# Optimization experiments

Measured on AMD Instinct MI355X. Metric: run time of the kernel, lower is better.

Reference implementation:

```python
import jax, jax.numpy as jnp
import numpy as np

N = 40000   # nodes
D = 128     # hidden_dim
R = 8       # num_rels
E = 640000  # edges (avg degree 16)
ND = 4000   # diseases (sim_matrix rows)


def setup_inputs() -> dict:
    key = jax.random.key(0)
    ks = jax.random.split(key, 9)
    s = 1.0 / np.sqrt(D)
    x = jax.random.normal(ks[0], (N, D), dtype=jnp.float32)
    edge_src = jax.random.randint(ks[1], (E,), 0, N, dtype=jnp.int32)
    edge_dst = jax.random.randint(ks[2], (E,), 0, N, dtype=jnp.int32)
    edge_type = jax.random.randint(ks[3], (E,), 0, R, dtype=jnp.int32)
    sim_matrix = jax.random.uniform(ks[4], (ND, ND), dtype=jnp.float32)
    # Full-batch case: batch_n_id = arange(N); diseases are ND unique global node ids.
    # The torch forward derives local positions + sim-matrix rows from global2local;
    # with identity batch ids this reduces to the sorted disease ids and arange(ND).
    rng = np.random.default_rng(0)
    disease_glob = np.sort(rng.choice(N, size=ND, replace=False))
    batch_loc_indices = jnp.asarray(disease_glob, dtype=jnp.int32)
    matrix_row_indices = jnp.arange(ND, dtype=jnp.int32)
    W1_self = jax.random.normal(ks[5], (D, D), dtype=jnp.float32) * s
    W1_rel = jax.random.normal(ks[6], (R, D, D), dtype=jnp.float32) * s
    W2_self = jax.random.normal(ks[7], (D, D), dtype=jnp.float32) * s
    W2_rel = jax.random.normal(ks[8], (R, D, D), dtype=jnp.float32) * s
    return {
        "x": x, "sim_matrix": sim_matrix,
        "W1_self": W1_self, "W1_rel": W1_rel,
        "W2_self": W2_self, "W2_rel": W2_rel,
        "edge_src": edge_src, "edge_dst": edge_dst, "edge_type": edge_type,
        "batch_loc_indices": batch_loc_indices,
        "matrix_row_indices": matrix_row_indices,
    }


def _rgcn_layer(h, src, dst, etype, Wself, Wrel):
    # Per-(dst, relation) mean aggregation of neighbor features, then per-relation GEMM.
    seg = dst * R + etype                                        # [E]
    msg = jax.ops.segment_sum(h[src], seg, num_segments=N * R)   # [N*R, D]
    cnt = jax.ops.segment_sum(jnp.ones((src.shape[0],), h.dtype), seg,
                              num_segments=N * R)                # [N*R]
    agg = (msg / jnp.maximum(cnt, 1.0)[:, None]).reshape(N, R, h.shape[1])
    return h @ Wself + jnp.einsum('nrd,rdh->nh', agg, Wrel)


def reference(x, sim_matrix, W1_self, W1_rel, W2_self, W2_rel,
              edge_src, edge_dst, edge_type, batch_loc_indices, matrix_row_indices):
    # --- RGCN encoder (2 layers) ---
    h = jax.nn.relu(_rgcn_layer(x, edge_src, edge_dst, edge_type, W1_self, W1_rel))
    h = _rgcn_layer(h, edge_src, edge_dst, edge_type, W2_self, W2_rel)

    # --- similarity diffusion post-processing ---
    deg = jax.ops.segment_sum(jnp.ones((edge_src.shape[0],), h.dtype),
                              edge_dst, num_segments=N)          # in-degree [N]
    c = 0.7 * jnp.exp(-0.7 * deg)[:, None] + 0.2                 # [N,1]

    hb = h[batch_loc_indices]                                    # [ND, D]
    sim_sub = sim_matrix[matrix_row_indices][:, matrix_row_indices]
    sim_norm = sim_sub / (sim_sub.sum(axis=1, keepdims=True) + 1e-9)
    h_sim = sim_norm @ hb                                        # [ND, D]

    c_sub = c[batch_loc_indices]
    h_aug = c_sub * h_sim + (1.0 - c_sub) * hb
    return h.at[batch_loc_indices].set(h_aug)
```

## Files before the change

### kernel.cpp

```cpp
#include <hip/hip_runtime.h>
#include <hip/hip_bf16.h>

#define DD 128
#define RR 8
#define KK 1152
#define SCAN_CHUNK 2048
#define KSPLIT 8
#define KP 4096

typedef _Float16 h8 __attribute__((ext_vector_type(8)));
typedef _Float16 h4 __attribute__((ext_vector_type(4)));
typedef float f4 __attribute__((ext_vector_type(4)));

__device__ __forceinline__ void gload16(const _Float16* g, _Float16* l) {
  __builtin_amdgcn_global_load_lds(
      (const __attribute__((address_space(1))) void*)g,
      (__attribute__((address_space(3))) void*)l, 16, 0, 0);
}

__global__ __launch_bounds__(256) void count_k(const int* __restrict__ edst,
    const int* __restrict__ etyp, int* __restrict__ cnt, int E) {
  int i = blockIdx.x * 256 + threadIdx.x;
  if (i < E) atomicAdd(&cnt[edst[i] * RR + etyp[i]], 1);
}

__global__ __launch_bounds__(256) void scan_a(const int* __restrict__ cnt,
    int* __restrict__ off, int* __restrict__ bsum, int n) {
  __shared__ int red[256];
  int base = blockIdx.x * SCAN_CHUNK + threadIdx.x * 8;
  int v[8];
  int s = 0;
#pragma unroll
  for (int i = 0; i < 8; ++i) {
    int idx = base + i;
    v[i] = s;
    s += (idx < n) ? cnt[idx] : 0;
  }
  red[threadIdx.x] = s;
  __syncthreads();
  for (int o = 1; o < 256; o <<= 1) {
    int t = (threadIdx.x >= o) ? red[threadIdx.x - o] : 0;
    __syncthreads();
    red[threadIdx.x] += t;
    __syncthreads();
  }
  int pre = (threadIdx.x > 0) ? red[threadIdx.x - 1] : 0;
#pragma unroll
  for (int i = 0; i < 8; ++i) {
    int idx = base + i;
    if (idx < n) off[idx] = v[i] + pre;
  }
  if (threadIdx.x == 255) bsum[blockIdx.x] = red[255];
}

__global__ void scan_b(int* __restrict__ bsum, int nb) {
  if (threadIdx.x == 0) {
    int s = 0;
    for (int i = 0; i < nb; ++i) { int t = bsum[i]; bsum[i] = s; s += t; }
  }
}

__global__ __launch_bounds__(256) void scan_c(int* __restrict__ off,
    const int* __restrict__ bsum, int n) {
  int i = blockIdx.x * 256 + threadIdx.x;
  if (i < n) off[i] += bsum[i >> 11];
}

__global__ __launch_bounds__(256) void fill_k(const int* __restrict__ esrc,
    const int* __restrict__ edst, const int* __restrict__ etyp,
    int* __restrict__ cur, int* __restrict__ eidx, int E) {
  int e = blockIdx.x * 256 + threadIdx.x;
  if (e < E) {
    int seg = edst[e] * RR + etyp[e];
    int p = atomicAdd(&cur[seg], 1);
    eidx[p] = esrc[e];
  }
}

__global__ __launch_bounds__(256) void convx_k(const float* __restrict__ x,
    _Float16* __restrict__ xh, int n4) {
  int i = blockIdx.x * 256 + threadIdx.x;
  if (i < n4) {
    float4 v = *(const float4*)(x + (size_t)i * 4);
    h4 o = {(_Float16)v.x, (_Float16)v.y, (_Float16)v.z, (_Float16)v.w};
    *(h4*)(xh + (size_t)i * 4) = o;
  }
}

__global__ __launch_bounds__(256) void convwT_k(const float* __restrict__ Ws,
    const float* __restrict__ Wr, _Float16* __restrict__ WT) {
  __shared__ _Float16 tile[64][72];
  const int k0 = blockIdx.x * 64, n0 = blockIdx.y * 64;
  const int t = threadIdx.x;
  {
    int kr = t >> 2, c0 = (t & 3) * 16;
    int k = k0 + kr;
    const float* src = (k < DD) ? (Ws + (size_t)k * DD + n0 + c0)
                                : (Wr + (size_t)(k - DD) * DD + n0 + c0);
#pragma unroll
    for (int j = 0; j < 16; j += 4) {
      float4 v = *(const float4*)(src + j);
      tile[kr][c0 + j + 0] = (_Float16)v.x;
      tile[kr][c0 + j + 1] = (_Float16)v.y;
      tile[kr][c0 + j + 2] = (_Float16)v.z;
      tile[kr][c0 + j + 3] = (_Float16)v.w;
    }
  }
  __syncthreads();
  {
    int nr = t >> 2, ck = (t & 3) * 16;
    h8 o0, o1;
#pragma unroll
    for (int j = 0; j < 8; ++j) {
      o0[j] = tile[ck + j][nr];
      o1[j] = tile[ck + 8 + j][nr];
    }
    *(h8*)(WT + (size_t)(n0 + nr) * KK + k0 + ck) = o0;
    *(h8*)(WT + (size_t)(n0 + nr) * KK + k0 + ck + 8) = o1;
  }
}

__device__ __forceinline__ void agg_body(const _Float16* __restrict__ h,
    const int* __restrict__ off, const int* __restrict__ eidx,
    _Float16* __restrict__ msg, int nseg, int E, int gid) {
  int seg = gid >> 4, q = gid & 15;
  if (seg >= nseg) return;
  int b = off[seg];
  int e = (seg + 1 < nseg) ? off[seg + 1] : E;
  int n = e - b;
  float a[8];
#pragma unroll
  for (int j = 0; j < 8; ++j) a[j] = 0.f;
  if (n > 0) {
    int e1 = e - 1;
    int s0 = eidx[b];
    int s1 = eidx[min(b + 1, e1)];
    int s2 = eidx[min(b + 2, e1)];
    int s3 = eidx[min(b + 3, e1)];
    h8 v0 = *(const h8*)(h + (size_t)s0 * DD + q * 8);
    h8 v1 = *(const h8*)(h + (size_t)s1 * DD + q * 8);
    h8 v2 = *(const h8*)(h + (size_t)s2 * DD + q * 8);
    h8 v3 = *(const h8*)(h + (size_t)s3 * DD + q * 8);
#pragma unroll
    for (int j = 0; j < 8; ++j) a[j] = (float)v0[j];
    if (n > 1) {
#pragma unroll
      for (int j = 0; j < 8; ++j) a[j] += (float)v1[j];
    }
    if (n > 2) {
#pragma unroll
      for (int j = 0; j < 8; ++j) a[j] += (float)v2[j];
    }
    if (n > 3) {
#pragma unroll
      for (int j = 0; j < 8; ++j) a[j] += (float)v3[j];
    }
    for (int i = b + 4; i < e; ++i) {
      int s = eidx[i];
      h8 v = *(const h8*)(h + (size_t)s * DD + q * 8);
#pragma unroll
      for (int j = 0; j < 8; ++j) a[j] += (float)v[j];
    }
  }
  float ic = (n > 0) ? 1.0f / (float)n : 0.0f;
  h8 o;
#pragma unroll
  for (int j = 0; j < 8; ++j) o[j] = (_Float16)(a[j] * ic);
  *(h8*)(msg + (size_t)seg * DD + q * 8) = o;
}

__global__ __launch_bounds__(256) void agg_k(const _Float16* __restrict__ h,
    const int* __restrict__ off, const int* __restrict__ eidx,
    _Float16* __restrict__ msg, int nseg, int E) {
  agg_body(h, off, eidx, msg, nseg, E, blockIdx.x * 256 + threadIdx.x);
}

__device__ __forceinline__ void convsim_body(const float* __restrict__ sim,
    const int* __restrict__ mri, const float* __restrict__ maskf,
    _Float16* __restrict__ simh, float* __restrict__ rs, int nd, int i,
    float* red) {
  const float* row = sim + (size_t)mri[i] * nd;
  float acc = 0.f;
  for (int c4 = threadIdx.x; c4 < KP / 4; c4 += 256) {
    int c = c4 * 4;
    float4 v = make_float4(0.f, 0.f, 0.f, 0.f);
    if (c < nd) {
      v = *(const float4*)(row + c);
      float4 mk = *(const float4*)(maskf + c);
      acc += v.x * mk.x + v.y * mk.y + v.z * mk.z + v.w * mk.w;
    }
    h4 o = {(_Float16)v.x, (_Float16)v.y, (_Float16)v.z, (_Float16)v.w};
    *(h4*)(simh + (size_t)i * KP + c) = o;
  }
  red[threadIdx.x] = acc;
  __syncthreads();
  for (int o = 128; o > 0; o >>= 1) {
    if (threadIdx.x < o) red[threadIdx.x] += red[threadIdx.x + o];
    __syncthreads();
  }
  if (threadIdx.x == 0) rs[i] = red[0] + 1e-9f;
}

__global__ __launch_bounds__(256) void agg1_convsim_k(
    const _Float16* __restrict__ h, const int* __restrict__ off,
    const int* __restrict__ eidx, _Float16* __restrict__ msg, int nseg, int E,
    const float* __restrict__ sim, const int* __restrict__ mri,
    const float* __restrict__ maskf, _Float16* __restrict__ simh,
    float* __restrict__ rs, int nd) {
  __shared__ float red[256];
  if ((int)blockIdx.x < nd) {
    convsim_body(sim, mri, maskf, simh, rs, nd, blockIdx.x, red);
  } else {
    agg_body(h, off, eidx, msg, nseg, E,
             (blockIdx.x - nd) * 256 + threadIdx.x);
  }
}

template <bool RELU, bool F16OUT>
__global__ __launch_bounds__(256) void rgcn_mfma(const _Float16* __restrict__ xh,
    const _Float16* __restrict__ msg, const _Float16* __restrict__ WT,
    void* __restrict__ outv, int nN) {
  __shared__ _Float16 Ab[2][64 * 64];
  __shared__ _Float16 Bb[2][128 * 64];
  const int t = threadIdx.x;
  const int lane = t & 63, w = t >> 6;
  const int row0 = blockIdx.x * 64;
  const int wm = w >> 1, wn = w & 1;
  const int lr = lane & 15, lg = lane >> 4;

  f4 acc[2][4];
#pragma unroll
  for (int mi = 0; mi < 2; ++mi)
#pragma unroll
    for (int ni = 0; ni < 4; ++ni) acc[mi][ni] = (f4){0.f, 0.f, 0.f, 0.f};

  const _Float16* pxh[2];
  const _Float16* pmsg[2];
  int ldsA[2];
#pragma unroll
  for (int j = 0; j < 2; ++j) {
    int q = j * 256 + w * 64 + lane;
    int row = q >> 3;
    int gck = (q & 7) ^ (row & 7);
    int m = row0 + row; if (m >= nN) m = nN - 1;
    pxh[j] = xh + (size_t)m * DD + gck * 8;
    pmsg[j] = msg + (size_t)m * (RR * DD) + gck * 8;
    ldsA[j] = (j * 256 + w * 64) * 8;
  }
  const _Float16* pB[4];
  int ldsB[4];
#pragma unroll
  for (int i = 0; i < 4; ++i) {
    int q = i * 256 + w * 64 + lane;
    int n = q >> 3;
    int gck = (q & 7) ^ (n & 7);
    pB[i] = WT + (size_t)n * KK + gck * 8;
    ldsB[i] = (i * 256 + w * 64) * 8;
  }

  const int nsteps = KK / 64;
#pragma unroll
  for (int j = 0; j < 2; ++j) gload16(pxh[j], &Ab[0][ldsA[j]]);
#pragma unroll
  for (int i = 0; i < 4; ++i) gload16(pB[i], &Bb[0][ldsB[i]]);
  asm volatile("s_waitcnt vmcnt(0)" ::: "memory");
  __syncthreads();

  for (int ts = 0; ts < nsteps; ++ts) {
    const int cur = ts & 1;
    if (ts + 1 < nsteps) {
      const int kk = (ts + 1) * 64;
      const int nxt = cur ^ 1;
      if (kk < DD) {
#pragma unroll
        for (int j = 0; j < 2; ++j) gload16(pxh[j] + kk, &Ab[nxt][ldsA[j]]);
      } else {
#pragma unroll
        for (int j = 0; j < 2; ++j) gload16(pmsg[j] + (kk - DD), &Ab[nxt][ldsA[j]]);
      }
#pragma unroll
      for (int i = 0; i < 4; ++i) gload16(pB[i] + kk, &Bb[nxt][ldsB[i]]);
    }
#pragma unroll
    for (int s = 0; s < 2; ++s) {
      h8 af[2], bf[4];
#pragma unroll
      for (int mi = 0; mi < 2; ++mi) {
        int r = wm * 32 + mi * 16 + lr;
        af[mi] = *(const h8*)&Ab[cur][r * 64 + (((s * 4 + lg) ^ (r & 7)) << 3)];
      }
#pragma unroll
      for (int ni = 0; ni < 4; ++ni) {
        int n = wn * 64 + ni * 16 + lr;
        bf[ni] = *(const h8*)&Bb[cur][n * 64 + (((s * 4 + lg) ^ (n & 7)) << 3)];
      }
#pragma unroll
      for (int mi = 0; mi < 2; ++mi)
#pragma unroll
        for (int ni = 0; ni < 4; ++ni)
          acc[mi][ni] = __builtin_amdgcn_mfma_f32_16x16x32_f16(
              af[mi], bf[ni], acc[mi][ni], 0, 0, 0);
    }
    asm volatile("s_waitcnt vmcnt(0)" ::: "memory");
    __syncthreads();
  }

#pragma unroll
  for (int mi = 0; mi < 2; ++mi) {
#pragma unroll
    for (int j = 0; j < 4; ++j) {
      int row = row0 + wm * 32 + mi * 16 + lg * 4 + j;
      if (row < nN) {
#pragma unroll
        for (int ni = 0; ni < 4; ++ni) {
          int col = wn * 64 + ni * 16 + lr;
          float v = acc[mi][ni][j];
          if (RELU) v = fmaxf(v, 0.f);
          if (F16OUT)
            ((_Float16*)outv)[(size_t)row * DD + col] = (_Float16)v;
          else
            ((float*)outv)[(size_t)row * DD + col] = v;
        }
      }
    }
  }
}

__global__ __launch_bounds__(256) void maskset_k(const int* __restrict__ mri,
    float* __restrict__ maskf, int nd) {
  int i = blockIdx.x * 256 + threadIdx.x;
  if (i < nd) maskf[mri[i]] = 1.0f;
}

__global__ __launch_bounds__(256) void gather2_k(const float* __restrict__ h2,
    const int* __restrict__ bli, const int* __restrict__ mri,
    float* __restrict__ hbp, _Float16* __restrict__ hbs, int nd) {
  int gid = blockIdx.x * 256 + threadIdx.x;
  int i = gid >> 5, q = gid & 31;
  if (i < nd) {
    float4 v = *(const float4*)(h2 + (size_t)bli[i] * DD + q * 4);
    *(float4*)(hbp + (size_t)i * DD + q * 4) = v;
    h4 o = {(_Float16)v.x, (_Float16)v.y, (_Float16)v.z, (_Float16)v.w};
    *(h4*)(hbs + (size_t)mri[i] * DD + q * 4) = o;
  }
}

__global__ __launch_bounds__(256) void transpose_k(const _Float16* __restrict__ hbs,
    _Float16* __restrict__ hbsT) {
  __shared__ _Float16 tile[64][72];
  int r0 = blockIdx.x * 64, c0 = blockIdx.y * 64;
  int t = threadIdx.x;
  int r = t >> 2, cs = (t & 3) * 16;
  *(h8*)&tile[r][cs]     = *(const h8*)(hbs + (size_t)(r0 + r) * DD + c0 + cs);
  *(h8*)&tile[r][cs + 8] = *(const h8*)(hbs + (size_t)(r0 + r) * DD + c0 + cs + 8);
  __syncthreads();
  int n = t >> 2, rs2 = (t & 3) * 16;
  h8 o0, o1;
#pragma unroll
  for (int j = 0; j < 8; ++j) {
    o0[j] = tile[rs2 + j][n];
    o1[j] = tile[rs2 + 8 + j][n];
  }
  *(h8*)(hbsT + (size_t)(c0 + n) * KP + r0 + rs2)     = o0;
  *(h8*)(hbsT + (size_t)(c0 + n) * KP + r0 + rs2 + 8) = o1;
}

__global__ __launch_bounds__(256) void sim_mfma(const _Float16* __restrict__ simh,
    const _Float16* __restrict__ hbsT, float* __restrict__ hs_part, int nd) {
  __shared__ _Float16 Ab[2][64 * 64];
  __shared__ _Float16 Bb[2][128 * 64];
  const int t = threadIdx.x;
  const int lane = t & 63, w = t >> 6;
  const int row0 = blockIdx.x * 64;
  const int kb0 = blockIdx.y * (KP / KSPLIT);
  const int wm = w >> 1, wn = w & 1;
  const int lr = lane & 15, lg = lane >> 4;

  f4 acc[2][4];
#pragma unroll
  for (int mi = 0; mi < 2; ++mi)
#pragma unroll
    for (int ni = 0; ni < 4; ++ni) acc[mi][ni] = (f4){0.f, 0.f, 0.f, 0.f};

  const _Float16* pA[2];
  int ldsA[2];
#pragma unroll
  for (int j = 0; j < 2; ++j) {
    int q = j * 256 + w * 64 + lane;
    int row = q >> 3;
    int gck = (q & 7) ^ (row & 7);
    int m = row0 + row; if (m >= nd) m = nd - 1;
    pA[j] = simh + (size_t)m * KP + kb0 + gck * 8;
    ldsA[j] = (j * 256 + w * 64) * 8;
  }
  const _Float16* pB[4];
  int ldsB[4];
#pragma unroll
  for (int i = 0; i < 4; ++i) {
    int q = i * 256 + w * 64 + lane;
    int n = q >> 3;
    int gck = (q & 7) ^ (n & 7);
    pB[i] = hbsT + (size_t)n * KP + kb0 + gck * 8;
    ldsB[i] = (i * 256 + w * 64) * 8;
  }

  const int nsteps = (KP / KSPLIT) / 64;
#pragma unroll
  for (int j = 0; j < 2; ++j) gload16(pA[j], &Ab[0][ldsA[j]]);
#pragma unroll
  for (int i = 0; i < 4; ++i) gload16(pB[i], &Bb[0][ldsB[i]]);
  asm volatile("s_waitcnt vmcnt(0)" ::: "memory");
  __syncthreads();

  for (int ts = 0; ts < nsteps; ++ts) {
    const int cur = ts & 1;
    if (ts + 1 < nsteps) {
      const int kk = (ts + 1) * 64;
      const int nxt = cur ^ 1;
#pragma unroll
      for (int j = 0; j < 2; ++j) gload16(pA[j] + kk, &Ab[nxt][ldsA[j]]);
#pragma unroll
      for (int i = 0; i < 4; ++i) gload16(pB[i] + kk, &Bb[nxt][ldsB[i]]);
    }
#pragma unroll
    for (int s = 0; s < 2; ++s) {
      h8 af[2], bf[4];
#pragma unroll
      for (int mi = 0; mi < 2; ++mi) {
        int r = wm * 32 + mi * 16 + lr;
        af[mi] = *(const h8*)&Ab[cur][r * 64 + (((s * 4 + lg) ^ (r & 7)) << 3)];
      }
#pragma unroll
      for (int ni = 0; ni < 4; ++ni) {
        int n = wn * 64 + ni * 16 + lr;
        bf[ni] = *(const h8*)&Bb[cur][n * 64 + (((s * 4 + lg) ^ (n & 7)) << 3)];
      }
#pragma unroll
      for (int mi = 0; mi < 2; ++mi)
#pragma unroll
        for (int ni = 0; ni < 4; ++ni)
          acc[mi][ni] = __builtin_amdgcn_mfma_f32_16x16x32_f16(
              af[mi], bf[ni], acc[mi][ni], 0, 0, 0);
    }
    asm volatile("s_waitcnt vmcnt(0)" ::: "memory");
    __syncthreads();
  }

  float* dst = hs_part + (size_t)blockIdx.y * nd * DD;
#pragma unroll
  for (int mi = 0; mi < 2; ++mi) {
#pragma unroll
    for (int j = 0; j < 4; ++j) {
      int row = row0 + wm * 32 + mi * 16 + lg * 4 + j;
      if (row < nd) {
#pragma unroll
        for (int ni = 0; ni < 4; ++ni) {
          int col = wn * 64 + ni * 16 + lr;
          dst[(size_t)row * DD + col] = acc[mi][ni][j];
        }
      }
    }
  }
}

__global__ __launch_bounds__(256) void reduce_final_k(
    const float* __restrict__ part, const float* __restrict__ hbp,
    const float* __restrict__ rs, const int* __restrict__ bli,
    const int* __restrict__ off, float* __restrict__ out, int nd,
    int NR, int E) {
  int gid = blockIdx.x * 256 + threadIdx.x;
  int i = gid >> 5, q = gid & 31;
  if (i < nd) {
    f4 s = (f4){0.f, 0.f, 0.f, 0.f};
#pragma unroll
    for (int p = 0; p < KSPLIT; ++p)
      s += *(const f4*)(part + (size_t)p * nd * DD + (size_t)i * DD + q * 4);
    int g = bli[i];
    int o0 = off[g * RR];
    int o1 = (g * RR + RR < NR) ? off[g * RR + RR] : E;
    float degf = (float)(o1 - o0);
    float cg = 0.7f * expf(-0.7f * degf) + 0.2f;
    float inv = 1.0f / rs[i];
    f4 bb = *(const f4*)(hbp + (size_t)i * DD + q * 4);
    f4 o;
#pragma unroll
    for (int j = 0; j < 4; ++j) o[j] = cg * (s[j] * inv) + (1.f - cg) * bb[j];
    *(f4*)(out + (size_t)g * DD + q * 4) = o;
  }
}

extern "C" void kernel_launch(void* const* d_in, const int* in_sizes, int n_in,
                              void* d_out, int out_size, void* d_ws, size_t ws_size,
                              hipStream_t stream) {
  const float* x   = (const float*)d_in[0];
  const float* sim = (const float*)d_in[1];
  const float* W1s = (const float*)d_in[2];
  const float* W1r = (const float*)d_in[3];
  const float* W2s = (const float*)d_in[4];
  const float* W2r = (const float*)d_in[5];
  const int* esrc  = (const int*)d_in[6];
  const int* edst  = (const int*)d_in[7];
  const int* etyp  = (const int*)d_in[8];
  const int* bli   = (const int*)d_in[9];
  const int* mri   = (const int*)d_in[10];
  const int N  = in_sizes[0] / DD;
  const int E  = in_sizes[6];
  const int ND = in_sizes[9];
  const int NR = N * RR;
  float* out = (float*)d_out;

  char* w = (char*)d_ws;
  _Float16* msg  = (_Float16*)w; w += (size_t)NR * DD * sizeof(_Float16);
  _Float16* xh   = (_Float16*)w; w += (size_t)N * DD * sizeof(_Float16);
  _Float16* h1h  = (_Float16*)w; w += (size_t)N * DD * sizeof(_Float16);
  _Float16* WT1  = (_Float16*)w; w += (size_t)DD * KK * sizeof(_Float16);
  _Float16* WT2  = (_Float16*)w; w += (size_t)DD * KK * sizeof(_Float16);
  _Float16* simh = (_Float16*)w; w += (size_t)ND * KP * sizeof(_Float16);
  _Float16* hbs  = (_Float16*)w; w += (size_t)KP * DD * sizeof(_Float16);
  _Float16* hbsT = (_Float16*)w; w += (size_t)DD * KP * sizeof(_Float16);
  float* hs_part = (float*)w; w += (size_t)KSPLIT * ND * DD * sizeof(float);
  float* hbp   = (float*)w; w += (size_t)ND * DD * sizeof(float);
  float* maskf = (float*)w; w += (size_t)KP * sizeof(float);
  int* cnt  = (int*)w; w += (size_t)NR * sizeof(int);
  int* off  = (int*)w; w += (size_t)NR * sizeof(int);
  int* cur  = (int*)w; w += (size_t)NR * sizeof(int);
  int* eidx = (int*)w; w += (size_t)E * sizeof(int);
  int* bsum = (int*)w; w += 1024 * sizeof(int);
  float* rs = (float*)w; w += (size_t)ND * sizeof(float);

  hipMemsetAsync(cnt, 0, (size_t)NR * sizeof(int), stream);
  count_k<<<(E + 255) / 256, 256, 0, stream>>>(edst, etyp, cnt, E);
  int nblk = (NR + SCAN_CHUNK - 1) / SCAN_CHUNK;
  scan_a<<<nblk, 256, 0, stream>>>(cnt, off, bsum, NR);
  scan_b<<<1, 256, 0, stream>>>(bsum, nblk);
  scan_c<<<(NR + 255) / 256, 256, 0, stream>>>(off, bsum, NR);
  hipMemcpyAsync(cur, off, (size_t)NR * sizeof(int), hipMemcpyDeviceToDevice, stream);
  fill_k<<<(E + 255) / 256, 256, 0, stream>>>(esrc, edst, etyp, cur, eidx, E);

  convx_k<<<(N * DD / 4 + 255) / 256, 256, 0, stream>>>(x, xh, N * DD / 4);
  dim3 wgrid(KK / 64, DD / 64);
  convwT_k<<<wgrid, 256, 0, stream>>>(W1s, W1r, WT1);
  convwT_k<<<wgrid, 256, 0, stream>>>(W2s, W2r, WT2);
  hipMemsetAsync(maskf, 0, (size_t)KP * sizeof(float), stream);
  maskset_k<<<(ND + 255) / 256, 256, 0, stream>>>(mri, maskf, ND);
  hipMemsetAsync(hbs, 0, (size_t)KP * DD * sizeof(_Float16), stream);

  int aggBlk = (NR * 16 + 255) / 256;
  agg1_convsim_k<<<ND + aggBlk, 256, 0, stream>>>(
      xh, off, eidx, msg, NR, E, sim, mri, maskf, simh, rs, ND);
  rgcn_mfma<true, true><<<(N + 63) / 64, 256, 0, stream>>>(xh, msg, WT1, h1h, N);

  agg_k<<<aggBlk, 256, 0, stream>>>(h1h, off, eidx, msg, NR, E);
  rgcn_mfma<false, false><<<(N + 63) / 64, 256, 0, stream>>>(h1h, msg, WT2, out, N);

  gather2_k<<<(ND * 32 + 255) / 256, 256, 0, stream>>>(out, bli, mri, hbp, hbs, ND);
  dim3 tgrid(KP / 64, DD / 64);
  transpose_k<<<tgrid, 256, 0, stream>>>(hbs, hbsT);
  dim3 sgrid((ND + 63) / 64, KSPLIT);
  sim_mfma<<<sgrid, 256, 0, stream>>>(simh, hbsT, hs_part, ND);
  reduce_final_k<<<(ND * 32 + 255) / 256, 256, 0, stream>>>(
      hs_part, hbp, rs, bli, off, out, ND, NR, E);
}
```

Before: 266.4 us.

## Merge preprocessing kernels into one launch and fold memsets and copy

Puts sim conversion, x conversion, both weight transposes and edge counting into a single block-partitioned prep kernel. The three memsets become one by making the buffers contiguous, and the offset-to-cursor memcpy is folded into scan_c. The first aggregation no longer shares a launch with sim conversion. The goal is fewer launches and serialization gaps, but the prep kernel now sits before the scan, so sim conversion no longer overlaps with layer-1 aggregation.

```diff
diff --git a/kernel.cpp b/kernel.cpp
--- a/kernel.cpp
+++ b/kernel.cpp
@@ -16,12 +16,6 @@
   __builtin_amdgcn_global_load_lds(
       (const __attribute__((address_space(1))) void*)g,
       (__attribute__((address_space(3))) void*)l, 16, 0, 0);
-}
-
-__global__ __launch_bounds__(256) void count_k(const int* __restrict__ edst,
-    const int* __restrict__ etyp, int* __restrict__ cnt, int E) {
-  int i = blockIdx.x * 256 + threadIdx.x;
-  if (i < E) atomicAdd(&cnt[edst[i] * RR + etyp[i]], 1);
 }
 
 __global__ __launch_bounds__(256) void scan_a(const int* __restrict__ cnt,
@@ -61,9 +55,13 @@
 }
 
 __global__ __launch_bounds__(256) void scan_c(int* __restrict__ off,
-    const int* __restrict__ bsum, int n) {
+    const int* __restrict__ bsum, int* __restrict__ cur, int n) {
   int i = blockIdx.x * 256 + threadIdx.x;
-  if (i < n) off[i] += bsum[i >> 11];
+  if (i < n) {
+    int v = off[i] + bsum[i >> 11];
+    off[i] = v;
+    cur[i] = v;
+  }
 }
 
 __global__ __launch_bounds__(256) void fill_k(const int* __restrict__ esrc,
@@ -77,102 +75,10 @@
   }
 }
 
-__global__ __launch_bounds__(256) void convx_k(const float* __restrict__ x,
-    _Float16* __restrict__ xh, int n4) {
+__global__ __launch_bounds__(256) void maskset_k(const int* __restrict__ mri,
+    float* __restrict__ maskf, int nd) {
   int i = blockIdx.x * 256 + threadIdx.x;
-  if (i < n4) {
-    float4 v = *(const float4*)(x + (size_t)i * 4);
-    h4 o = {(_Float16)v.x, (_Float16)v.y, (_Float16)v.z, (_Float16)v.w};
-    *(h4*)(xh + (size_t)i * 4) = o;
-  }
-}
-
-__global__ __launch_bounds__(256) void convwT_k(const float* __restrict__ Ws,
-    const float* __restrict__ Wr, _Float16* __restrict__ WT) {
-  __shared__ _Float16 tile[64][72];
-  const int k0 = blockIdx.x * 64, n0 = blockIdx.y * 64;
-  const int t = threadIdx.x;
-  {
-    int kr = t >> 2, c0 = (t & 3) * 16;
-    int k = k0 + kr;
-    const float* src = (k < DD) ? (Ws + (size_t)k * DD + n0 + c0)
-                                : (Wr + (size_t)(k - DD) * DD + n0 + c0);
-#pragma unroll
-    for (int j = 0; j < 16; j += 4) {
-      float4 v = *(const float4*)(src + j);
-      tile[kr][c0 + j + 0] = (_Float16)v.x;
-      tile[kr][c0 + j + 1] = (_Float16)v.y;
-      tile[kr][c0 + j + 2] = (_Float16)v.z;
-      tile[kr][c0 + j + 3] = (_Float16)v.w;
-    }
-  }
-  __syncthreads();
-  {
-    int nr = t >> 2, ck = (t & 3) * 16;
-    h8 o0, o1;
-#pragma unroll
-    for (int j = 0; j < 8; ++j) {
-      o0[j] = tile[ck + j][nr];
-      o1[j] = tile[ck + 8 + j][nr];
-    }
-    *(h8*)(WT + (size_t)(n0 + nr) * KK + k0 + ck) = o0;
-    *(h8*)(WT + (size_t)(n0 + nr) * KK + k0 + ck + 8) = o1;
-  }
-}
-
-__device__ __forceinline__ void agg_body(const _Float16* __restrict__ h,
-    const int* __restrict__ off, const int* __restrict__ eidx,
-    _Float16* __restrict__ msg, int nseg, int E, int gid) {
-  int seg = gid >> 4, q = gid & 15;
-  if (seg >= nseg) return;
-  int b = off[seg];
-  int e = (seg + 1 < nseg) ? off[seg + 1] : E;
-  int n = e - b;
-  float a[8];
-#pragma unroll
-  for (int j = 0; j < 8; ++j) a[j] = 0.f;
-  if (n > 0) {
-    int e1 = e - 1;
-    int s0 = eidx[b];
-    int s1 = eidx[min(b + 1, e1)];
-    int s2 = eidx[min(b + 2, e1)];
-    int s3 = eidx[min(b + 3, e1)];
-    h8 v0 = *(const h8*)(h + (size_t)s0 * DD + q * 8);
-    h8 v1 = *(const h8*)(h + (size_t)s1 * DD + q * 8);
-    h8 v2 = *(const h8*)(h + (size_t)s2 * DD + q * 8);
-    h8 v3 = *(const h8*)(h + (size_t)s3 * DD + q * 8);
-#pragma unroll
-    for (int j = 0; j < 8; ++j) a[j] = (float)v0[j];
-    if (n > 1) {
-#pragma unroll
-      for (int j = 0; j < 8; ++j) a[j] += (float)v1[j];
-    }
-    if (n > 2) {
-#pragma unroll
-      for (int j = 0; j < 8; ++j) a[j] += (float)v2[j];
-    }
-    if (n > 3) {
-#pragma unroll
-      for (int j = 0; j < 8; ++j) a[j] += (float)v3[j];
-    }
-    for (int i = b + 4; i < e; ++i) {
-      int s = eidx[i];
-      h8 v = *(const h8*)(h + (size_t)s * DD + q * 8);
-#pragma unroll
-      for (int j = 0; j < 8; ++j) a[j] += (float)v[j];
-    }
-  }
-  float ic = (n > 0) ? 1.0f / (float)n : 0.0f;
-  h8 o;
-#pragma unroll
-  for (int j = 0; j < 8; ++j) o[j] = (_Float16)(a[j] * ic);
-  *(h8*)(msg + (size_t)seg * DD + q * 8) = o;
-}
-
-__global__ __launch_bounds__(256) void agg_k(const _Float16* __restrict__ h,
-    const int* __restrict__ off, const int* __restrict__ eidx,
-    _Float16* __restrict__ msg, int nseg, int E) {
-  agg_body(h, off, eidx, msg, nseg, E, blockIdx.x * 256 + threadIdx.x);
+  if (i < nd) maskf[mri[i]] = 1.0f;
 }
 
 __device__ __forceinline__ void convsim_body(const float* __restrict__ sim,
@@ -201,19 +107,136 @@
   if (threadIdx.x == 0) rs[i] = red[0] + 1e-9f;
 }
 
-__global__ __launch_bounds__(256) void agg1_convsim_k(
-    const _Float16* __restrict__ h, const int* __restrict__ off,
-    const int* __restrict__ eidx, _Float16* __restrict__ msg, int nseg, int E,
+__device__ __forceinline__ void convwT_body(const float* __restrict__ Ws,
+    const float* __restrict__ Wr, _Float16* __restrict__ WT, int bid,
+    _Float16 (*tile)[72]) {
+  const int k0 = (bid % (KK / 64)) * 64, n0 = (bid / (KK / 64)) * 64;
+  const int t = threadIdx.x;
+  {
+    int kr = t >> 2, c0 = (t & 3) * 16;
+    int k = k0 + kr;
+    const float* src = (k < DD) ? (Ws + (size_t)k * DD + n0 + c0)
+                                : (Wr + (size_t)(k - DD) * DD + n0 + c0);
+#pragma unroll
+    for (int j = 0; j < 16; j += 4) {
+      float4 v = *(const float4*)(src + j);
+      tile[kr][c0 + j + 0] = (_Float16)v.x;
+      tile[kr][c0 + j + 1] = (_Float16)v.y;
+      tile[kr][c0 + j + 2] = (_Float16)v.z;
+      tile[kr][c0 + j + 3] = (_Float16)v.w;
+    }
+  }
+  __syncthreads();
+  {
+    int nr = t >> 2, ck = (t & 3) * 16;
+    h8 o0, o1;
+#pragma unroll
+    for (int j = 0; j < 8; ++j) {
+      o0[j] = tile[ck + j][nr];
+      o1[j] = tile[ck + 8 + j][nr];
+    }
+    *(h8*)(WT + (size_t)(n0 + nr) * KK + k0 + ck) = o0;
+    *(h8*)(WT + (size_t)(n0 + nr) * KK + k0 + ck + 8) = o1;
+  }
+}
+
+__global__ __launch_bounds__(256) void prep_k(
     const float* __restrict__ sim, const int* __restrict__ mri,
     const float* __restrict__ maskf, _Float16* __restrict__ simh,
-    float* __restrict__ rs, int nd) {
-  __shared__ float red[256];
-  if ((int)blockIdx.x < nd) {
-    convsim_body(sim, mri, maskf, simh, rs, nd, blockIdx.x, red);
-  } else {
-    agg_body(h, off, eidx, msg, nseg, E,
-             (blockIdx.x - nd) * 256 + threadIdx.x);
-  }
+    float* __restrict__ rs, int nd,
+    const float* __restrict__ x, _Float16* __restrict__ xh, int n4x,
+    const float* __restrict__ W1s, const float* __restrict__ W1r,
+    _Float16* __restrict__ WT1,
+    const float* __restrict__ W2s, const float* __restrict__ W2r,
+    _Float16* __restrict__ WT2,
+    const int* __restrict__ edst, const int* __restrict__ etyp,
+    int* __restrict__ cnt, int E, int bX, int bW) {
+  __shared__ char smem[64 * 72 * 2];
+  const int b = blockIdx.x, t = threadIdx.x;
+  if (b < nd) {
+    convsim_body(sim, mri, maskf, simh, rs, nd, b, (float*)smem);
+    return;
+  }
+  int b2 = b - nd;
+  if (b2 < bX) {
+    int i = b2 * 256 + t;
+    if (i < n4x) {
+      float4 v = *(const float4*)(x + (size_t)i * 4);
+      h4 o = {(_Float16)v.x, (_Float16)v.y, (_Float16)v.z, (_Float16)v.w};
+      *(h4*)(xh + (size_t)i * 4) = o;
+    }
+    return;
+  }
+  b2 -= bX;
+  if (b2 < bW) {
+    convwT_body(W1s, W1r, WT1, b2, (_Float16(*)[72])smem);
+    return;
+  }
+  b2 -= bW;
+  if (b2 < bW) {
+    convwT_body(W2s, W2r, WT2, b2, (_Float16(*)[72])smem);
+    return;
+  }
+  b2 -= bW;
+  {
+    int i = b2 * 256 + t;
+    if (i < E) atomicAdd(&cnt[edst[i] * RR + etyp[i]], 1);
+  }
+}
+
+__device__ __forceinline__ void agg_body(const _Float16* __restrict__ h,
+    const int* __restrict__ off, const int* __restrict__ eidx,
+    _Float16* __restrict__ msg, int nseg, int E, int gid) {
+  int seg = gid >> 4, q = gid & 15;
+  if (seg >= nseg) return;
+  int b = off[seg];
+  int e = (seg + 1 < nseg) ? off[seg + 1] : E;
+  int n = e - b;
+  float a[8];
+#pragma unroll
+  for (int j = 0; j < 8; ++j) a[j] = 0.f;
+  if (n > 0) {
+    int e1 = e - 1;
+    int s0 = eidx[b];
+    int s1 = eidx[min(b + 1, e1)];
+    int s2 = eidx[min(b + 2, e1)];
+    int s3 = eidx[min(b + 3, e1)];
+    h8 v0 = *(const h8*)(h + (size_t)s0 * DD + q * 8);
+    h8 v1 = *(const h8*)(h + (size_t)s1 * DD + q * 8);
+    h8 v2 = *(const h8*)(h + (size_t)s2 * DD + q * 8);
+    h8 v3 = *(const h8*)(h + (size_t)s3 * DD + q * 8);
+#pragma unroll
+    for (int j = 0; j < 8; ++j) a[j] = (float)v0[j];
+    if (n > 1) {
+#pragma unroll
+      for (int j = 0; j < 8; ++j) a[j] += (float)v1[j];
+    }
+    if (n > 2) {
+#pragma unroll
+      for (int j = 0; j < 8; ++j) a[j] += (float)v2[j];
+    }
+    if (n > 3) {
+#pragma unroll
+      for (int j = 0; j < 8; ++j) a[j] += (float)v3[j];
+    }
+    for (int i = b + 4; i < e; ++i) {
+      int s = eidx[i];
+      h8 v = *(const h8*)(h + (size_t)s * DD + q * 8);
+#pragma unroll
+      for (int j = 0; j < 8; ++j) a[j] += (float)v[j];
+    }
+  }
+  float ic = (n > 0) ? 1.0f / (float)n : 0.0f;
+  h8 o;
+#pragma unroll
+  for (int j = 0; j < 8; ++j) o[j] = (_Float16)(a[j] * ic);
+  *(h8*)(msg + (size_t)seg * DD + q * 8) = o;
+}
+
+__global__ __launch_bounds__(256) void agg_k(const _Float16* __restrict__ h,
+    const int* __restrict__ off, const int* __restrict__ eidx,
+    _Float16* __restrict__ msg, int nseg, int E) {
+  agg_body(h, off, eidx, msg, nseg, E, blockIdx.x * 256 + threadIdx.x);
 }
 
 template <bool RELU, bool F16OUT>
@@ -324,12 +347,6 @@
       }
     }
   }
-}
-
-__global__ __launch_bounds__(256) void maskset_k(const int* __restrict__ mri,
-    float* __restrict__ maskf, int nd) {
-  int i = blockIdx.x * 256 + threadIdx.x;
-  if (i < nd) maskf[mri[i]] = 1.0f;
 }
 
 __global__ __launch_bounds__(256) void gather2_k(const float* __restrict__ h2,
@@ -516,38 +533,39 @@
   _Float16* WT1  = (_Float16*)w; w += (size_t)DD * KK * sizeof(_Float16);
   _Float16* WT2  = (_Float16*)w; w += (size_t)DD * KK * sizeof(_Float16);
   _Float16* simh = (_Float16*)w; w += (size_t)ND * KP * sizeof(_Float16);
-  _Float16* hbs  = (_Float16*)w; w += (size_t)KP * DD * sizeof(_Float16);
   _Float16* hbsT = (_Float16*)w; w += (size_t)DD * KP * sizeof(_Float16);
   float* hs_part = (float*)w; w += (size_t)KSPLIT * ND * DD * sizeof(float);
   float* hbp   = (float*)w; w += (size_t)ND * DD * sizeof(float);
-  float* maskf = (float*)w; w += (size_t)KP * sizeof(float);
-  int* cnt  = (int*)w; w += (size_t)NR * sizeof(int);
+  int* cnt       = (int*)w;      w += (size_t)NR * sizeof(int);
+  float* maskf   = (float*)w;    w += (size_t)KP * sizeof(float);
+  _Float16* hbs  = (_Float16*)w; w += (size_t)KP * DD * sizeof(_Float16);
   int* off  = (int*)w; w += (size_t)NR * sizeof(int);
   int* cur  = (int*)w; w += (size_t)NR * sizeof(int);
   int* eidx = (int*)w; w += (size_t)E * sizeof(int);
   int* bsum = (int*)w; w += 1024 * sizeof(int);
   float* rs = (float*)w; w += (size_t)ND * sizeof(float);
 
-  hipMemsetAsync(cnt, 0, (size_t)NR * sizeof(int), stream);
-  count_k<<<(E + 255) / 256, 256, 0, stream>>>(edst, etyp, cnt, E);
+  const size_t zbytes = (size_t)NR * sizeof(int) + (size_t)KP * sizeof(float) +
+                        (size_t)KP * DD * sizeof(_Float16);
+  hipMemsetAsync(cnt, 0, zbytes, stream);
+  maskset_k<<<(ND + 255) / 256, 256, 0, stream>>>(mri, maskf, ND);
+
+  const int n4x = N * DD / 4;
+  const int bX = (n4x + 255) / 256;
+  const int bW = (KK / 64) * (DD / 64);
+  const int bC = (E + 255) / 256;
+  prep_k<<<ND + bX + 2 * bW + bC, 256, 0, stream>>>(
+      sim, mri, maskf, simh, rs, ND, x, xh, n4x,
+      W1s, W1r, WT1, W2s, W2r, WT2, edst, etyp, cnt, E, bX, bW);
+
   int nblk = (NR + SCAN_CHUNK - 1) / SCAN_CHUNK;
   scan_a<<<nblk, 256, 0, stream>>>(cnt, off, bsum, NR);
   scan_b<<<1, 256, 0, stream>>>(bsum, nblk);
-  scan_c<<<(NR + 255) / 256, 256, 0, stream>>>(off, bsum, NR);
-  hipMemcpyAsync(cur, off, (size_t)NR * sizeof(int), hipMemcpyDeviceToDevice, stream);
-  fill_k<<<(E + 255) / 256, 256, 0, stream>>>(esrc, edst, etyp, cur, eidx, E);
-
-  convx_k<<<(N * DD / 4 + 255) / 256, 256, 0, stream>>>(x, xh, N * DD / 4);
-  dim3 wgrid(KK / 64, DD / 64);
-  convwT_k<<<wgrid, 256, 0, stream>>>(W1s, W1r, WT1);
-  convwT_k<<<wgrid, 256, 0, stream>>>(W2s, W2r, WT2);
-  hipMemsetAsync(maskf, 0, (size_t)KP * sizeof(float), stream);
-  maskset_k<<<(ND + 255) / 256, 256, 0, stream>>>(mri, maskf, ND);
-  hipMemsetAsync(hbs, 0, (size_t)KP * DD * sizeof(_Float16), stream);
+  scan_c<<<(NR + 255) / 256, 256, 0, stream>>>(off, bsum, cur, NR);
+  fill_k<<<bC, 256, 0, stream>>>(esrc, edst, etyp, cur, eidx, E);
 
   int aggBlk = (NR * 16 + 255) / 256;
-  agg1_convsim_k<<<ND + aggBlk, 256, 0, stream>>>(
-      xh, off, eidx, msg, NR, E, sim, mri, maskf, simh, rs, ND);
+  agg_k<<<aggBlk, 256, 0, stream>>>(xh, off, eidx, msg, NR, E);
   rgcn_mfma<true, true><<<(N + 63) / 64, 256, 0, stream>>>(xh, msg, WT1, h1h, N);
 
   agg_k<<<aggBlk, 256, 0, stream>>>(h1h, off, eidx, msg, NR, E);
```

Measured after the change: 252.8 us. 5.1% less time.
